# Kernel optimization log

Hardware: AMD Instinct MI355X
Metric: run time of the kernel (lower is better)

## Reference

```python
import jax, jax.numpy as jnp
import numpy as np

DIM = 2560; HEADS = 20; HEAD_DIM = 128
N_EXP = 4; TOP_K = 2; HID = 6912; SHID = 3584
B = 1; S = 2048
EPS = 1e-6


def setup_inputs():
    key = jax.random.key(0)
    ks = jax.random.split(key, 16)
    r = lambda i, shape, s=0.02: jax.random.normal(ks[i], shape, jnp.float32) * s
    # rope as [1,S,1,HD/2,2,2] rotation matrices: [[cos,-sin],[sin,cos]]
    ang = jax.random.uniform(ks[0], (1, S, 1, HEAD_DIM // 2), jnp.float32) * (2.0 * np.pi)
    c, s_ = jnp.cos(ang), jnp.sin(ang)
    rope = jnp.stack([jnp.stack([c, -s_], -1), jnp.stack([s_, c], -1)], -2)
    return dict(
        hidden_states=jax.random.normal(ks[1], (B, S, DIM), jnp.float32),
        temb=jax.random.normal(ks[2], (B, DIM), jnp.float32),
        rope=rope,
        adaln_w=r(3, (6 * DIM, DIM)), adaln_b=jnp.zeros((6 * DIM,), jnp.float32),
        qkv_w=r(4, (3 * DIM, DIM)), qkv_b=jnp.zeros((3 * DIM,), jnp.float32),
        qn_w=jnp.ones((DIM,), jnp.float32), kn_w=jnp.ones((DIM,), jnp.float32),
        out_w=r(5, (DIM, DIM)), out_b=jnp.zeros((DIM,), jnp.float32),
        gate_w=r(6, (N_EXP, DIM), 1.0 / DIM ** 0.5),
        ew1=r(7, (N_EXP, HID, DIM)), ew2=r(8, (N_EXP, DIM, HID)), ew3=r(9, (N_EXP, HID, DIM)),
        sw1=r(10, (SHID, DIM)), sw2=r(11, (DIM, SHID)), sw3=r(12, (SHID, DIM)),
    )


def _layernorm(x):  # elementwise_affine=False, eps=1e-6
    m = x.mean(-1, keepdims=True)
    v = ((x - m) ** 2).mean(-1, keepdims=True)
    return (x - m) * jax.lax.rsqrt(v + EPS)


def _rmsnorm(x, w):  # DistributedRMSNorm, tp_size=1
    return x * jax.lax.rsqrt((x ** 2).mean(-1, keepdims=True) + EPS) * w


def _apply_rope(x, rope):  # x:[B,S,H,D], rope:[1,S,1,D/2,2,2]
    b, s, h, d = x.shape
    x_ = x.reshape(b, s, h, d // 2, 1, 2)
    out = rope[..., 0] * x_[..., 0] + rope[..., 1] * x_[..., 1]  # [B,S,H,D/2,2]
    return out.reshape(b, s, h, d)


def _swiglu(x, w1, w2, w3):
    return (jax.nn.silu(x @ w1.T) * (x @ w3.T)) @ w2.T


def _forward(hidden_states, temb, rope, adaln_w, adaln_b, qkv_w, qkv_b, qn_w, kn_w,
             out_w, out_b, gate_w, ew1, ew2, ew3, sw1, sw2, sw3):
    b, s, d = hidden_states.shape
    # adaLN modulation: SiLU -> Linear -> [:, None] -> chunk(6)
    mod = (jax.nn.silu(temb) @ adaln_w.T + adaln_b)[:, None, :]
    shift_msa, scale_msa, gate_msa, shift_mlp, scale_mlp, gate_mlp = jnp.split(mod, 6, axis=-1)
    # --- attention ---
    nh = _layernorm(hidden_states) * (1.0 + scale_msa) + shift_msa
    qkv = nh @ qkv_w.T + qkv_b
    q, k, v = jnp.split(qkv, 3, axis=-1)  # each [B,S,inner_dim]
    q = _rmsnorm(q, qn_w)  # RMS over full inner_dim (all heads)
    k = _rmsnorm(k, kn_w)
    q = q.reshape(b, s, HEADS, HEAD_DIM)
    k = k.reshape(b, s, HEADS, HEAD_DIM)
    v = v.reshape(b, s, HEADS, HEAD_DIM)
    q = _apply_rope(q, rope)
    k = _apply_rope(k, rope)
    attn = jnp.einsum('bqhd,bkhd->bhqk', q, k) * (HEAD_DIM ** -0.5)
    attn = jax.nn.softmax(attn, axis=-1)
    o = jnp.einsum('bhqk,bkhd->bqhd', attn, v).reshape(b, s, HEADS * HEAD_DIM)
    o = o @ out_w.T + out_b
    hidden_states = gate_msa * o + hidden_states
    # --- MoE SwiGLU feed-forward ---
    nh = _layernorm(hidden_states) * (1.0 + scale_mlp) + shift_mlp
    x = nh.reshape(-1, d)  # [T,d]
    scores = jax.nn.softmax(x @ gate_w.T, axis=-1)  # [T,E]
    tw, ti = jax.lax.top_k(scores, TOP_K)  # norm_topk_prob=False
    t = x.shape[0]
    wdense = jnp.zeros((t, N_EXP), x.dtype).at[jnp.arange(t)[:, None], ti].set(tw)
    y = jnp.zeros_like(x)
    for e in range(N_EXP):  # fixed small expert count
        y = y + wdense[:, e:e + 1] * _swiglu(x, ew1[e], ew2[e], ew3[e])
    y = y.reshape(b, s, d) + _swiglu(nh, sw1, sw2, sw3)  # shared experts on identity
    return gate_mlp * y + hidden_states


def reference(hidden_states, temb, rope, adaln_w, adaln_b, qkv_w, qkv_b, qn_w, kn_w,
              out_w, out_b, gate_w, ew1, ew2, ew3, sw1, sw2, sw3):
    return _forward(hidden_states, temb, rope, adaln_w, adaln_b, qkv_w, qkv_b, qn_w, kn_w,
                    out_w, out_b, gate_w, ew1, ew2, ew3, sw1, sw2, sw3)
```

## Files before the change

kernel.cpp:

```cpp
#include <hip/hip_runtime.h>

#define DIM 2560
#define T_TOK 2048
#define NHEADS 20
#define HD 128
#define HID_E 6912
#define SHID_E 3584
#define MPAD 5120

typedef _Float16 f16x8 __attribute__((ext_vector_type(8)));
typedef float f32x4 __attribute__((ext_vector_type(4)));
typedef unsigned short u16x8 __attribute__((ext_vector_type(8)));

#define MFMA16(a, b, c) __builtin_amdgcn_mfma_f32_16x16x32_f16((a), (b), (c), 0, 0, 0)

__device__ inline unsigned short f2h(float f) {
  return __builtin_bit_cast(unsigned short, (_Float16)f);
}
__device__ inline float h2f(unsigned short u) {
  return (float)__builtin_bit_cast(_Float16, u);
}
__device__ inline float wave_sum(float v) {
#pragma unroll
  for (int off = 32; off > 0; off >>= 1) v += __shfl_down(v, off, 64);
  return v;
}
__device__ inline void gld16(const void* g, void* l) {
  __builtin_amdgcn_global_load_lds((const __attribute__((address_space(1))) void*)g,
                                   (__attribute__((address_space(3))) void*)l, 16, 0, 0);
}


__global__ __launch_bounds__(256) void silu_k(const float* __restrict__ t,
                                              float* __restrict__ ss) {
  int i = blockIdx.x * 256 + threadIdx.x;
  if (i < DIM) {
    float v = t[i];
    ss[i] = v / (1.f + expf(-v));
  }
}

__global__ __launch_bounds__(256) void cvt_all2(
    const float* __restrict__ s0, unsigned short* __restrict__ d0, long n0,
    const float* __restrict__ s1, unsigned short* __restrict__ d1, long n1) {
  const long stride = (long)gridDim.x * 256;
  const long tot = n0 + n1;
  for (long i = (long)blockIdx.x * 256 + threadIdx.x; i < tot; i += stride) {
    const float* s;
    unsigned short* d;
    long j;
    if (i < n0) { s = s0; d = d0; j = i; }
    else { s = s1; d = d1; j = i - n0; }
    float4 a = *(const float4*)(s + j * 8);
    float4 b = *(const float4*)(s + j * 8 + 4);
    u16x8 u;
    u[0] = f2h(a.x); u[1] = f2h(a.y); u[2] = f2h(a.z); u[3] = f2h(a.w);
    u[4] = f2h(b.x); u[5] = f2h(b.y); u[6] = f2h(b.z); u[7] = f2h(b.w);
    *(u16x8*)&d[j * 8] = u;
  }
}

__global__ __launch_bounds__(256) void adaln_gemv(const float* __restrict__ ss,
                                                  const float* __restrict__ W,
                                                  const float* __restrict__ bias,
                                                  float* __restrict__ mod) {
  const int lane = threadIdx.x & 63;
  const int j = blockIdx.x * 4 + (threadIdx.x >> 6);
  const float* wr = W + (size_t)j * DIM;
  float p = 0.f;
  for (int i = lane; i < 640; i += 64) {
    float4 w = *(const float4*)(wr + i * 4);
    float4 x = *(const float4*)(ss + i * 4);
    p += w.x * x.x + w.y * x.y + w.z * x.z + w.w * x.w;
  }
  p = wave_sum(p);
  if (lane == 0) mod[j] = p + bias[j];
}

__global__ __launch_bounds__(256) void ln_mod(const float* __restrict__ x,
                                              const float* __restrict__ shift,
                                              const float* __restrict__ scale,
                                              unsigned short* __restrict__ outp) {
  __shared__ float rbuf[8];
  const int t = blockIdx.x, tid = threadIdx.x, lane = tid & 63, wid = tid >> 6;
  const float* xr = x + (size_t)t * DIM;
  float s = 0.f, sq = 0.f;
  for (int i = tid; i < 640; i += 256) {
    float4 v = *(const float4*)(xr + i * 4);
    s += v.x + v.y + v.z + v.w;
    sq += v.x * v.x + v.y * v.y + v.z * v.z + v.w * v.w;
  }
  s = wave_sum(s);
  sq = wave_sum(sq);
  if (lane == 0) {
    rbuf[wid] = s;
    rbuf[4 + wid] = sq;
  }
  __syncthreads();
  float S = rbuf[0] + rbuf[1] + rbuf[2] + rbuf[3];
  float SQ = rbuf[4] + rbuf[5] + rbuf[6] + rbuf[7];
  float mean = S * (1.f / DIM);
  float rs = rsqrtf(SQ * (1.f / DIM) - mean * mean + 1e-6f);
  for (int i = tid; i < 640; i += 256) {
    float4 v = *(const float4*)(xr + i * 4);
    float4 sc4 = *(const float4*)(scale + i * 4);
    float4 sh4 = *(const float4*)(shift + i * 4);
    ushort4 u;
    u.x = f2h((v.x - mean) * rs * (1.f + sc4.x) + sh4.x);
    u.y = f2h((v.y - mean) * rs * (1.f + sc4.y) + sh4.y);
    u.z = f2h((v.z - mean) * rs * (1.f + sc4.z) + sh4.z);
    u.w = f2h((v.w - mean) * rs * (1.f + sc4.w) + sh4.w);
    *(ushort4*)&outp[(size_t)t * DIM + i * 4] = u;
  }
}

__global__ __launch_bounds__(256) void rmsrope(const unsigned short* __restrict__ qkv,
                                               const float* __restrict__ qn,
                                               const float* __restrict__ kn,
                                               const float* __restrict__ rope,
                                               unsigned short* __restrict__ qh,
                                               unsigned short* __restrict__ kh) {
  __shared__ float rbuf[8];
  const int t = blockIdx.x, tid = threadIdx.x, lane = tid & 63, wid = tid >> 6;
  const unsigned short* row = qkv + (size_t)t * 7680;
  float sq = 0.f, sk = 0.f;
  for (int i = tid; i < 320; i += 256) {
    f16x8 qv = *(const f16x8*)(row + i * 8);
    f16x8 kv = *(const f16x8*)(row + DIM + i * 8);
#pragma unroll
    for (int j = 0; j < 8; ++j) {
      float q = (float)qv[j], k = (float)kv[j];
      sq += q * q;
      sk += k * k;
    }
  }
  sq = wave_sum(sq);
  sk = wave_sum(sk);
  if (lane == 0) {
    rbuf[wid] = sq;
    rbuf[4 + wid] = sk;
  }
  __syncthreads();
  float SQ = rbuf[0] + rbuf[1] + rbuf[2] + rbuf[3];
  float SK = rbuf[4] + rbuf[5] + rbuf[6] + rbuf[7];
  float rq = rsqrtf(SQ * (1.f / DIM) + 1e-6f) * 0.08838834764831845f;
  float rk = rsqrtf(SK * (1.f / DIM) + 1e-6f);
  for (int pp = tid; pp < 1280; pp += 256) {
    int c = pp * 2;
    float qe = h2f(row[c]) * rq * qn[c], qo = h2f(row[c + 1]) * rq * qn[c + 1];
    float ke = h2f(row[DIM + c]) * rk * kn[c], ko = h2f(row[DIM + c + 1]) * rk * kn[c + 1];
    float4 rr = *(const float4*)(rope + (size_t)t * 256 + (pp & 63) * 4);
    unsigned qp = (unsigned)f2h(rr.x * qe + rr.y * qo) |
                  ((unsigned)f2h(rr.z * qe + rr.w * qo) << 16);
    unsigned kp = (unsigned)f2h(rr.x * ke + rr.y * ko) |
                  ((unsigned)f2h(rr.z * ke + rr.w * ko) << 16);
    *(unsigned*)&qh[(size_t)t * DIM + c] = qp;
    *(unsigned*)&kh[(size_t)t * DIM + c] = kp;
  }
}

__global__ void transpose_v(const unsigned short* __restrict__ in,
                            unsigned short* __restrict__ outp) {
  __shared__ unsigned short tile[32][33];
  const int bx = blockIdx.x * 32;
  const int by = blockIdx.y * 32;
  const int tx = threadIdx.x, ty = threadIdx.y;
  for (int j = ty; j < 32; j += 8)
    tile[j][tx] = in[(size_t)(by + j) * 7680 + 5120 + bx + tx];
  __syncthreads();
  for (int j = ty; j < 32; j += 8)
    outp[(size_t)(bx + j) * T_TOK + by + tx] = tile[tx][j];
}

__global__ __launch_bounds__(256) void fattn(const unsigned short* __restrict__ qh,
                                             const unsigned short* __restrict__ kh,
                                             const unsigned short* __restrict__ vt,
                                             unsigned short* __restrict__ obuf) {
  __shared__ unsigned short sK[64 * 128];
  __shared__ unsigned short sV[128 * 64];
  __shared__ unsigned short sP[64 * 64];
  __shared__ float sRedM[4][64];
  __shared__ float sRedL[4][64];
  __shared__ float sM[64];
  __shared__ float sL[64];
  const int tid = threadIdx.x, lane = tid & 63, wv = tid >> 6;
  const int g = lane >> 4, fr = lane & 15;
  const int h = blockIdx.y;
  const int q0 = blockIdx.x * 64;

  {
    const int r = tid >> 2, qt = tid & 3;
    const unsigned short* gp = qh + (size_t)(q0 + r) * DIM + h * HD + qt * 32;
    uint4 v0 = ((const uint4*)gp)[0];
    uint4 v1 = ((const uint4*)gp)[1];
    uint4 v2 = ((const uint4*)gp)[2];
    uint4 v3 = ((const uint4*)gp)[3];
    unsigned short* dst = &sK[r * 128];
    const int cb = qt * 4, rs = r & 15;
    *(uint4*)&dst[((cb + 0) ^ rs) * 8] = v0;
    *(uint4*)&dst[((cb + 1) ^ rs) * 8] = v1;
    *(uint4*)&dst[((cb + 2) ^ rs) * 8] = v2;
    *(uint4*)&dst[((cb + 3) ^ rs) * 8] = v3;
  }
  __syncthreads();
  f16x8 qfrag[4][4];
#pragma unroll
  for (int ni = 0; ni < 4; ++ni) {
#pragma unroll
    for (int kt = 0; kt < 4; ++kt) {
      int r = ni * 16 + fr;
      qfrag[ni][kt] = *(const f16x8*)&sK[r * 128 + (((kt * 4 + g) ^ (r & 15)) << 3)];
    }
  }
  __syncthreads();

  f32x4 acco[4][2];
  f32x4 mprev[4];
  float mrun[4], lrun[4];
#pragma unroll
  for (int i = 0; i < 4; ++i) {
    acco[i][0] = (f32x4)0.f;
    acco[i][1] = (f32x4)0.f;
    mprev[i] = (f32x4)(-1e30f);
    mrun[i] = -1e30f;
    lrun[i] = 0.f;
  }

  for (int kt0 = 0; kt0 < T_TOK; kt0 += 64) {
    {
      const int r = tid >> 2, qt = tid & 3;
      const unsigned short* gp = kh + (size_t)(kt0 + r) * DIM + h * HD + qt * 32;
      uint4 v0 = ((const uint4*)gp)[0];
      uint4 v1 = ((const uint4*)gp)[1];
      uint4 v2 = ((const uint4*)gp)[2];
      uint4 v3 = ((const uint4*)gp)[3];
      unsigned short* dst = &sK[r * 128];
      const int cb = qt * 4, rs = r & 15;
      *(uint4*)&dst[((cb + 0) ^ rs) * 8] = v0;
      *(uint4*)&dst[((cb + 1) ^ rs) * 8] = v1;
      *(uint4*)&dst[((cb + 2) ^ rs) * 8] = v2;
      *(uint4*)&dst[((cb + 3) ^ rs) * 8] = v3;
      const int rv = tid >> 1, hf = tid & 1;
      const unsigned short* gv = vt + (size_t)(h * HD + rv) * T_TOK + kt0 + hf * 32;
      uint4 w0 = ((const uint4*)gv)[0];
      uint4 w1 = ((const uint4*)gv)[1];
      uint4 w2 = ((const uint4*)gv)[2];
      uint4 w3 = ((const uint4*)gv)[3];
      unsigned short* dv = &sV[rv * 64];
      const int cv = hf * 4, rvs = rv & 7;
      *(uint4*)&dv[((cv + 0) ^ rvs) * 8] = w0;
      *(uint4*)&dv[((cv + 1) ^ rvs) * 8] = w1;
      *(uint4*)&dv[((cv + 2) ^ rvs) * 8] = w2;
      *(uint4*)&dv[((cv + 3) ^ rvs) * 8] = w3;
    }
    __syncthreads();

    f32x4 accs[4] = {(f32x4)0.f, (f32x4)0.f, (f32x4)0.f, (f32x4)0.f};
#pragma unroll
    for (int kt = 0; kt < 4; ++kt) {
      int r = wv * 16 + fr;
      f16x8 ak = *(const f16x8*)&sK[r * 128 + (((kt * 4 + g) ^ (r & 15)) << 3)];
#pragma unroll
      for (int ni = 0; ni < 4; ++ni) accs[ni] = MFMA16(ak, qfrag[ni][kt], accs[ni]);
    }

    float pm[4];
#pragma unroll
    for (int ni = 0; ni < 4; ++ni) {
      float m = fmaxf(fmaxf(accs[ni][0], accs[ni][1]), fmaxf(accs[ni][2], accs[ni][3]));
      m = fmaxf(m, __shfl_xor(m, 16));
      m = fmaxf(m, __shfl_xor(m, 32));
      pm[ni] = m;
    }
    if (g == 0) {
#pragma unroll
      for (int ni = 0; ni < 4; ++ni) sRedM[wv][ni * 16 + fr] = pm[ni];
    }
    __syncthreads();
    float mnew[4];
#pragma unroll
    for (int ni = 0; ni < 4; ++ni) {
      int q = ni * 16 + fr;
      float mt = fmaxf(fmaxf(sRedM[0][q], sRedM[1][q]), fmaxf(sRedM[2][q], sRedM[3][q]));
      mnew[ni] = fmaxf(mrun[ni], mt);
    }
    float lsum[4];
#pragma unroll
    for (int ni = 0; ni < 4; ++ni) {
      float l0 = 0.f;
#pragma unroll
      for (int i = 0; i < 4; ++i) {
        float p = __expf(accs[ni][i] - mnew[ni]);
        accs[ni][i] = p;
        l0 += p;
      }
      l0 += __shfl_xor(l0, 16);
      l0 += __shfl_xor(l0, 32);
      lsum[ni] = l0;
    }
    if (g == 0) {
#pragma unroll
      for (int ni = 0; ni < 4; ++ni) sRedL[wv][ni * 16 + fr] = lsum[ni];
      if (wv == 0) {
#pragma unroll
        for (int ni = 0; ni < 4; ++ni) sM[ni * 16 + fr] = mnew[ni];
      }
    }
#pragma unroll
    for (int ni = 0; ni < 4; ++ni) {
      int q = ni * 16 + fr;
      unsigned p01 = (unsigned)f2h(accs[ni][0]) | ((unsigned)f2h(accs[ni][1]) << 16);
      unsigned p23 = (unsigned)f2h(accs[ni][2]) | ((unsigned)f2h(accs[ni][3]) << 16);
      uint2 pk;
      pk.x = p01;
      pk.y = p23;
      *(uint2*)&sP[q * 64 + ((((wv << 1) | (g >> 1)) ^ (q & 7)) << 3) + ((g & 1) << 2)] = pk;
    }
    __syncthreads();
#pragma unroll
    for (int ni = 0; ni < 4; ++ni) {
      int q = ni * 16 + fr;
      float lt = sRedL[0][q] + sRedL[1][q] + sRedL[2][q] + sRedL[3][q];
      lrun[ni] = lrun[ni] * __expf(mrun[ni] - mnew[ni]) + lt;
      mrun[ni] = mnew[ni];
    }

#pragma unroll
    for (int mi = 0; mi < 4; ++mi) {
      f32x4 mn = *(const f32x4*)&sM[mi * 16 + g * 4];
      f32x4 sc;
#pragma unroll
      for (int i = 0; i < 4; ++i) sc[i] = __expf(mprev[mi][i] - mn[i]);
      acco[mi][0] *= sc;
      acco[mi][1] *= sc;
      mprev[mi] = mn;
    }
#pragma unroll
    for (int ktp = 0; ktp < 2; ++ktp) {
      f16x8 bv[2];
#pragma unroll
      for (int nd = 0; nd < 2; ++nd) {
        int r = wv * 32 + nd * 16 + fr;
        bv[nd] = *(const f16x8*)&sV[r * 64 + (((ktp * 4 + g) ^ (r & 7)) << 3)];
      }
#pragma unroll
      for (int mi = 0; mi < 4; ++mi) {
        int r = mi * 16 + fr;
        f16x8 ap = *(const f16x8*)&sP[r * 64 + (((ktp * 4 + g) ^ (r & 7)) << 3)];
        acco[mi][0] = MFMA16(ap, bv[0], acco[mi][0]);
        acco[mi][1] = MFMA16(ap, bv[1], acco[mi][1]);
      }
    }
    __syncthreads();
  }

  if (wv == 0 && g == 0) {
#pragma unroll
    for (int ni = 0; ni < 4; ++ni) sL[ni * 16 + fr] = 1.f / lrun[ni];
  }
  __syncthreads();
#pragma unroll
  for (int mi = 0; mi < 4; ++mi) {
    f32x4 li = *(const f32x4*)&sL[mi * 16 + g * 4];
#pragma unroll
    for (int nd = 0; nd < 2; ++nd) {
#pragma unroll
      for (int i = 0; i < 4; ++i) {
        float o = acco[mi][nd][i] * li[i];
        obuf[(size_t)(q0 + mi * 16 + g * 4 + i) * DIM + h * HD + wv * 32 + nd * 16 + fr] =
            f2h(o);
      }
    }
  }
}

__global__ __launch_bounds__(256) void ln2_route(const float* __restrict__ x,
                                                 const float* __restrict__ shift,
                                                 const float* __restrict__ scale,
                                                 const float* __restrict__ gw,
                                                 unsigned short* __restrict__ nh2,
                                                 float* __restrict__ wd) {
  __shared__ float rbuf[8];
  __shared__ float gbuf[4][4];
  const int t = blockIdx.x, tid = threadIdx.x, lane = tid & 63, wid = tid >> 6;
  const float* xr = x + (size_t)t * DIM;
  float s = 0.f, sq = 0.f;
  for (int i = tid; i < 640; i += 256) {
    float4 v = *(const float4*)(xr + i * 4);
    s += v.x + v.y + v.z + v.w;
    sq += v.x * v.x + v.y * v.y + v.z * v.z + v.w * v.w;
  }
  s = wave_sum(s);
  sq = wave_sum(sq);
  if (lane == 0) {
    rbuf[wid] = s;
    rbuf[4 + wid] = sq;
  }
  __syncthreads();
  float S = rbuf[0] + rbuf[1] + rbuf[2] + rbuf[3];
  float SQ = rbuf[4] + rbuf[5] + rbuf[6] + rbuf[7];
  float mean = S * (1.f / DIM);
  float rs = rsqrtf(SQ * (1.f / DIM) - mean * mean + 1e-6f);
  float g0 = 0.f, g1 = 0.f, g2 = 0.f, g3 = 0.f;
  for (int i = tid; i < 640; i += 256) {
    float4 v = *(const float4*)(xr + i * 4);
    float4 sc4 = *(const float4*)(scale + i * 4);
    float4 sh4 = *(const float4*)(shift + i * 4);
    float y0 = (v.x - mean) * rs * (1.f + sc4.x) + sh4.x;
    float y1 = (v.y - mean) * rs * (1.f + sc4.y) + sh4.y;
    float y2 = (v.z - mean) * rs * (1.f + sc4.z) + sh4.z;
    float y3 = (v.w - mean) * rs * (1.f + sc4.w) + sh4.w;
    ushort4 u;
    u.x = f2h(y0); u.y = f2h(y1); u.z = f2h(y2); u.w = f2h(y3);
    *(ushort4*)&nh2[(size_t)t * DIM + i * 4] = u;
    float4 w0 = *(const float4*)(gw + i * 4);
    float4 w1 = *(const float4*)(gw + DIM + i * 4);
    float4 w2 = *(const float4*)(gw + 2 * DIM + i * 4);
    float4 w3 = *(const float4*)(gw + 3 * DIM + i * 4);
    g0 += y0 * w0.x + y1 * w0.y + y2 * w0.z + y3 * w0.w;
    g1 += y0 * w1.x + y1 * w1.y + y2 * w1.z + y3 * w1.w;
    g2 += y0 * w2.x + y1 * w2.y + y2 * w2.z + y3 * w2.w;
    g3 += y0 * w3.x + y1 * w3.y + y2 * w3.z + y3 * w3.w;
  }
  g0 = wave_sum(g0);
  g1 = wave_sum(g1);
  g2 = wave_sum(g2);
  g3 = wave_sum(g3);
  if (lane == 0) {
    gbuf[wid][0] = g0; gbuf[wid][1] = g1; gbuf[wid][2] = g2; gbuf[wid][3] = g3;
  }
  __syncthreads();
  if (tid == 0) {
    float l[4];
#pragma unroll
    for (int e = 0; e < 4; ++e) l[e] = gbuf[0][e] + gbuf[1][e] + gbuf[2][e] + gbuf[3][e];
    float mx = fmaxf(fmaxf(l[0], l[1]), fmaxf(l[2], l[3]));
    float ex[4], sum = 0.f;
#pragma unroll
    for (int e = 0; e < 4; ++e) { ex[e] = expf(l[e] - mx); sum += ex[e]; }
    float p[4];
#pragma unroll
    for (int e = 0; e < 4; ++e) p[e] = ex[e] / sum;
    int i1 = 0;
    for (int e = 1; e < 4; ++e)
      if (p[e] > p[i1]) i1 = e;
    int i2 = -1;
    for (int e = 0; e < 4; ++e) {
      if (e == i1) continue;
      if (i2 < 0 || p[e] > p[i2]) i2 = e;
    }
    float w[4] = {0.f, 0.f, 0.f, 0.f};
    w[i1] = p[i1];
    w[i2] = p[i2];
    *(float4*)&wd[(size_t)t * 4] = make_float4(w[0], w[1], w[2], w[3]);
  }
}

__global__ __launch_bounds__(256) void route_compact(const float* __restrict__ wd,
                                                     int* __restrict__ idx_all,
                                                     int* __restrict__ seg,
                                                     int* __restrict__ slotAB,
                                                     float* __restrict__ wAB) {
  __shared__ unsigned short c[256][4];
  __shared__ int offs[256][4];
  __shared__ int segs[5];
  const int t = threadIdx.x;
  for (int i = t; i < MPAD; i += 256) idx_all[i] = 0;
  unsigned char sel[8];
  float wv4[8][4];
  unsigned short lc[4] = {0, 0, 0, 0};
#pragma unroll
  for (int k = 0; k < 8; ++k) {
    int tok = t * 8 + k;
    float4 w = *(const float4*)&wd[(size_t)tok * 4];
    wv4[k][0] = w.x; wv4[k][1] = w.y; wv4[k][2] = w.z; wv4[k][3] = w.w;
    unsigned m = 0;
    if (w.x != 0.f) { m |= 1; lc[0]++; }
    if (w.y != 0.f) { m |= 2; lc[1]++; }
    if (w.z != 0.f) { m |= 4; lc[2]++; }
    if (w.w != 0.f) { m |= 8; lc[3]++; }
    sel[k] = (unsigned char)m;
  }
#pragma unroll
  for (int e = 0; e < 4; ++e) c[t][e] = lc[e];
  __syncthreads();
  if (t == 0) {
    int run[4] = {0, 0, 0, 0};
    for (int i = 0; i < 256; ++i) {
#pragma unroll
      for (int e = 0; e < 4; ++e) {
        offs[i][e] = run[e];
        run[e] += c[i][e];
      }
    }
    int s = 0;
    segs[0] = 0;
#pragma unroll
    for (int e = 0; e < 4; ++e) {
      s += (run[e] + 255) & ~255;
      segs[e + 1] = s;
    }
#pragma unroll
    for (int e = 0; e < 5; ++e) seg[e] = segs[e];
  }
  __syncthreads();
  int o[4];
#pragma unroll
  for (int e = 0; e < 4; ++e) o[e] = segs[e] + offs[t][e];
#pragma unroll
  for (int k = 0; k < 8; ++k) {
    int tok = t * 8 + k;
    unsigned m = sel[k];
    int sl[2] = {0, 0};
    float sw[2] = {0.f, 0.f};
    int ns = 0;
#pragma unroll
    for (int e = 0; e < 4; ++e) {
      if ((m >> e) & 1) {
        if (ns < 2) { sl[ns] = o[e]; sw[ns] = wv4[k][e]; }
        idx_all[o[e]++] = tok;
        ns++;
      }
    }
    if (ns == 1) { sl[1] = sl[0]; sw[1] = 0.f; }
    slotAB[tok * 2] = sl[0];
    slotAB[tok * 2 + 1] = sl[1];
    wAB[tok * 2] = sw[0];
    wAB[tok * 2 + 1] = sw[1];
  }
}

template <int EPI, int MODE>
__global__ __launch_bounds__(256) void gemm128(
    const unsigned short* __restrict__ A, const unsigned short* __restrict__ B,
    const float* __restrict__ bias, void* __restrict__ Cv,
    const float* __restrict__ aux0, const float* __restrict__ aux1,
    const int* __restrict__ idx, const int* __restrict__ seg,
    const int* __restrict__ slotAB, const float* __restrict__ wAB,
    const unsigned short* __restrict__ yc, int M, int N, int K) {
  __shared__ unsigned short smem[16384];
  const int tid = threadIdx.x;
  const int lane = tid & 63;
  const int wv = tid >> 6;
  const int nwg = gridDim.x;
  const int bid = blockIdx.x;
  const int swzb = (bid & 7) * (nwg >> 3) + (bid >> 3);
  const int gm = M >> 7;
  const int m0 = (swzb % gm) * 128, n0 = (swzb / gm) * 128;
  if (MODE != 0 && m0 >= seg[4]) return;

  const unsigned short* Bp = B;
  if constexpr (MODE != 0) {
    int e = 0;
#pragma unroll
    for (int i = 1; i < 4; ++i)
      if (m0 >= seg[i]) e = i;
    Bp = B + (size_t)e * N * K;
  }

  const int wm = (wv >> 1) * 64, wn = (wv & 1) * 64;
  const int fr = lane & 15, fc = lane >> 4;

  const int rl = lane >> 2, ch = lane & 3;
  const int R1 = wv * 16 + rl;
  const int R2 = 64 + R1;
  const int co1 = ((ch ^ ((R1 >> 1) & 3)) << 3);
  const int co2 = ((ch ^ ((R2 >> 1) & 3)) << 3);
  const size_t ar1 = (size_t)(m0 + R1) * K;
  const size_t ar2 = (size_t)(m0 + R2) * K;
  const unsigned short* gA1 = A + ar1 + co1;
  const unsigned short* gA2 = A + ar2 + co2;
  const unsigned short* gB1 = Bp + (size_t)(n0 + R1) * K + co1;
  const unsigned short* gB2 = Bp + (size_t)(n0 + R2) * K + co2;
  const int lA1 = (wv * 16) * 32, lA2 = (64 + wv * 16) * 32;

  f32x4 acc[4][4];
#pragma unroll
  for (int i = 0; i < 4; ++i) {
#pragma unroll
    for (int j = 0; j < 4; ++j) acc[i][j] = (f32x4)0.f;
  }

  auto STAGE = [&](int buf, int kt) {
    unsigned short* base = smem + buf * 8192;
    gld16(gA1 + kt, base + lA1);
    gld16(gA2 + kt, base + lA2);
    gld16(gB1 + kt, base + 4096 + lA1);
    gld16(gB2 + kt, base + 4096 + lA2);
  };
  auto COMPUTE = [&](int buf) {
    const unsigned short* sA = smem + buf * 8192;
    const unsigned short* sB = sA + 4096;
    f16x8 a[4], b[4];
#pragma unroll
    for (int mi = 0; mi < 4; ++mi) {
      int r = wm + mi * 16 + fr;
      a[mi] = *(const f16x8*)&sA[r * 32 + ((fc ^ ((r >> 1) & 3)) << 3)];
    }
#pragma unroll
    for (int ni = 0; ni < 4; ++ni) {
      int r = wn + ni * 16 + fr;
      b[ni] = *(const f16x8*)&sB[r * 32 + ((fc ^ ((r >> 1) & 3)) << 3)];
    }
#pragma unroll
    for (int mi = 0; mi < 4; ++mi) {
#pragma unroll
      for (int ni = 0; ni < 4; ++ni) acc[mi][ni] = MFMA16(a[mi], b[ni], acc[mi][ni]);
    }
  };

  const int nk = K >> 5;
  STAGE(0, 0);
  __syncthreads();
  int cur = 0;
  for (int t = 1; t < nk; ++t) {
    STAGE(cur ^ 1, t << 5);
    COMPUTE(cur);
    __syncthreads();
    cur ^= 1;
  }
  COMPUTE(cur);

#pragma unroll
  for (int mi = 0; mi < 4; ++mi) {
#pragma unroll
    for (int ni = 0; ni < 4; ++ni) {
      const int n = n0 + wn + ni * 16 + fr;
      const int mb = m0 + wm + mi * 16 + fc * 4;
#pragma unroll
      for (int i = 0; i < 4; ++i) {
        const int m = mb + i;
        float v = acc[mi][ni][i];
        const size_t cidx = (size_t)m * N + n;
        if constexpr (EPI == 1) {
          ((float*)Cv)[cidx] = aux0[n] * (v + bias[n]) + aux1[cidx];
        } else if constexpr (EPI == 4) {
          if (bias) v += bias[n];
          ((unsigned short*)Cv)[cidx] = f2h(v);
        } else if constexpr (EPI == 6) {
          const int sA_ = slotAB[m * 2], sB_ = slotAB[m * 2 + 1];
          const float wA_ = wAB[m * 2], wB_ = wAB[m * 2 + 1];
          float vm = wA_ * h2f(yc[(size_t)sA_ * N + n]) + wB_ * h2f(yc[(size_t)sB_ * N + n]);
          ((float*)Cv)[cidx] = aux0[n] * (v + vm) + aux1[cidx];
        }
      }
    }
  }
}

template <int EPI, int MODE, int PAIR>
__global__ __launch_bounds__(512) void gemm256(
    const unsigned short* __restrict__ A, const float* __restrict__ B1,
    const float* __restrict__ B3, const float* __restrict__ bias,
    void* __restrict__ Cv, const int* __restrict__ idx, const int* __restrict__ seg,
    int M, int N, int K) {
  __shared__ __align__(16) char smem[147456];
  const int tid = threadIdx.x;
  const int lane = tid & 63;
  const int wv = tid >> 6;
  const int wr = wv >> 2;
  const int wc = wv & 3;
  const int fr = lane & 15, fc = lane >> 4;

  const int nwg = gridDim.x;
  const int bid = blockIdx.x;
  const int swzb = (bid & 7) * (nwg >> 3) + (bid >> 3);
  const int gm = M >> 8;
  const int m0 = (swzb % gm) * 256, n0 = (swzb / gm) * 256;
  if (MODE != 0 && m0 >= seg[4]) return;

  const float* B1p = B1;
  const float* B3p = B3;
  if constexpr (MODE != 0) {
    int e = 0;
#pragma unroll
    for (int i = 1; i < 4; ++i)
      if (m0 >= seg[i]) e = i;
    if constexpr (PAIR) {
      B1p = B1 + (size_t)e * (N >> 1) * K;
      B3p = B3 + (size_t)e * (N >> 1) * K;
    } else {
      B1p = B1 + (size_t)e * N * K;
    }
  }

  const int srowA = lane >> 2;
  const int sccA = ((lane & 3) ^ ((lane >> 3) & 3)) << 3;
  int mr0, mr1;
  if constexpr (MODE == 1) {
    mr0 = idx[m0 + wv * 16 + srowA];
    mr1 = idx[m0 + 128 + wv * 16 + srowA];
  } else {
    mr0 = m0 + wv * 16 + srowA;
    mr1 = m0 + 128 + wv * 16 + srowA;
  }
  const unsigned short* gA0 = A + (size_t)mr0 * K + sccA;
  const unsigned short* gA1 = A + (size_t)mr1 * K + sccA;

  const int srowB = lane >> 3;
  const int sccB = ((lane & 7) ^ srowB) << 2;
  const float* gB[4];
#pragma unroll
  for (int s = 0; s < 4; ++s) {
    const int rB = n0 + wv * 32 + s * 8 + srowB;
    const float* bsrc;
    if constexpr (PAIR) {
      const float* mptr = ((rB >> 4) & 1) ? B3p : B1p;
      bsrc = mptr + (size_t)((rB >> 5) * 16 + (rB & 15)) * K;
    } else {
      bsrc = B1p + (size_t)rB * K;
    }
    gB[s] = bsrc + sccB;
  }

  const int swA_ = (fr >> 1) & 3;
  const int foA = ((fc ^ swA_) << 3);
  const int aoff = (wr * 128 + fr) * 32 + foA;
  const int mB = fr & 7;
  const int bc0 = ((2 * fc) ^ mB) << 2;
  const int bc1 = ((2 * fc + 1) ^ mB) << 2;

  f32x4 acc[8][4];
#pragma unroll
  for (int i = 0; i < 8; ++i) {
#pragma unroll
    for (int j = 0; j < 4; ++j) acc[i][j] = (f32x4)0.f;
  }

  auto STAGE_A = [&](int buf, int kt) {
    char* bb = smem + buf * 49152;
    gld16(gA0 + kt, bb + wv * 1024);
    gld16(gA1 + kt, bb + 8192 + wv * 1024);
  };
  auto STAGE_B = [&](int buf, int kt) {
    char* bb = smem + buf * 49152 + 16384 + wv * 4096;
#pragma unroll
    for (int s = 0; s < 4; ++s) gld16(gB[s] + kt, bb + s * 1024);
  };

  const int nk = K >> 5;
  STAGE_A(0, 0);
  STAGE_B(0, 0);
  STAGE_A(1, 32);
  STAGE_B(1, 32);

  int cur = 0;
  for (int t = 0; t < nk; ++t) {
    if (t < nk - 1)
      asm volatile("s_waitcnt vmcnt(6)" ::: "memory");
    else
      asm volatile("s_waitcnt vmcnt(0)" ::: "memory");
    __builtin_amdgcn_s_barrier();
    __builtin_amdgcn_sched_barrier(0);

    const unsigned short* sA = (const unsigned short*)(smem + cur * 49152);
    const float* sB = (const float*)(smem + cur * 49152 + 16384);
    int nxt = cur + 2;
    if (nxt >= 3) nxt -= 3;
    const bool more = (t + 2) < nk;
    const int kn = (t + 2) << 5;

    f16x8 bfr[4];
#pragma unroll
    for (int ni = 0; ni < 4; ++ni) {
      const float* rowp = sB + (wc * 64 + ni * 16 + fr) * 32;
      float4 x = *(const float4*)&rowp[bc0];
      float4 y = *(const float4*)&rowp[bc1];
      f16x8 b;
      b[0] = (_Float16)x.x; b[1] = (_Float16)x.y; b[2] = (_Float16)x.z; b[3] = (_Float16)x.w;
      b[4] = (_Float16)y.x; b[5] = (_Float16)y.y; b[6] = (_Float16)y.z; b[7] = (_Float16)y.w;
      bfr[ni] = b;
    }
    f16x8 b0 = bfr[0], b1 = bfr[1], b2 = bfr[2], b3 = bfr[3];

    {
      f16x8 a0 = *(const f16x8*)&sA[aoff];
      f16x8 a1 = *(const f16x8*)&sA[aoff + 512];
      if (more) STAGE_A(nxt, kn);
      __builtin_amdgcn_sched_barrier(0);
      __builtin_amdgcn_s_setprio(1);
      acc[0][0] = MFMA16(a0, b0, acc[0][0]);
      acc[0][1] = MFMA16(a0, b1, acc[0][1]);
      acc[0][2] = MFMA16(a0, b2, acc[0][2]);
      acc[0][3] = MFMA16(a0, b3, acc[0][3]);
      acc[1][0] = MFMA16(a1, b0, acc[1][0]);
      acc[1][1] = MFMA16(a1, b1, acc[1][1]);
      acc[1][2] = MFMA16(a1, b2, acc[1][2]);
      acc[1][3] = MFMA16(a1, b3, acc[1][3]);
      __builtin_amdgcn_s_setprio(0);
      __builtin_amdgcn_sched_barrier(0);
    }
    {
      f16x8 a0 = *(const f16x8*)&sA[aoff + 1024];
      f16x8 a1 = *(const f16x8*)&sA[aoff + 1536];
      if (more) STAGE_B(nxt, kn);
      __builtin_amdgcn_sched_barrier(0);
      __builtin_amdgcn_s_setprio(1);
      acc[2][0] = MFMA16(a0, b0, acc[2][0]);
      acc[2][1] = MFMA16(a0, b1, acc[2][1]);
      acc[2][2] = MFMA16(a0, b2, acc[2][2]);
      acc[2][3] = MFMA16(a0, b3, acc[2][3]);
      acc[3][0] = MFMA16(a1, b0, acc[3][0]);
      acc[3][1] = MFMA16(a1, b1, acc[3][1]);
      acc[3][2] = MFMA16(a1, b2, acc[3][2]);
      acc[3][3] = MFMA16(a1, b3, acc[3][3]);
      __builtin_amdgcn_s_setprio(0);
      __builtin_amdgcn_sched_barrier(0);
    }
    {
      f16x8 a0 = *(const f16x8*)&sA[aoff + 2048];
      f16x8 a1 = *(const f16x8*)&sA[aoff + 2560];
      __builtin_amdgcn_sched_barrier(0);
      __builtin_amdgcn_s_setprio(1);
      acc[4][0] = MFMA16(a0, b0, acc[4][0]);
      acc[4][1] = MFMA16(a0, b1, acc[4][1]);
      acc[4][2] = MFMA16(a0, b2, acc[4][2]);
      acc[4][3] = MFMA16(a0, b3, acc[4][3]);
      acc[5][0] = MFMA16(a1, b0, acc[5][0]);
      acc[5][1] = MFMA16(a1, b1, acc[5][1]);
      acc[5][2] = MFMA16(a1, b2, acc[5][2]);
      acc[5][3] = MFMA16(a1, b3, acc[5][3]);
      __builtin_amdgcn_s_setprio(0);
      __builtin_amdgcn_sched_barrier(0);
    }
    {
      f16x8 a0 = *(const f16x8*)&sA[aoff + 3072];
      f16x8 a1 = *(const f16x8*)&sA[aoff + 3584];
      __builtin_amdgcn_sched_barrier(0);
      __builtin_amdgcn_s_setprio(1);
      acc[6][0] = MFMA16(a0, b0, acc[6][0]);
      acc[6][1] = MFMA16(a0, b1, acc[6][1]);
      acc[6][2] = MFMA16(a0, b2, acc[6][2]);
      acc[6][3] = MFMA16(a0, b3, acc[6][3]);
      acc[7][0] = MFMA16(a1, b0, acc[7][0]);
      acc[7][1] = MFMA16(a1, b1, acc[7][1]);
      acc[7][2] = MFMA16(a1, b2, acc[7][2]);
      acc[7][3] = MFMA16(a1, b3, acc[7][3]);
      __builtin_amdgcn_s_setprio(0);
      __builtin_amdgcn_sched_barrier(0);
    }
    cur += 1;
    if (cur >= 3) cur -= 3;
  }

  if constexpr (EPI == 5) {
    unsigned short* Ch = (unsigned short*)Cv;
    const int Nh = N >> 1;
#pragma unroll
    for (int mi = 0; mi < 8; ++mi) {
#pragma unroll
      for (int p = 0; p < 2; ++p) {
        const int hcol = (((n0 + wc * 64) >> 5) + p) * 16 + fr;
        const int mb = m0 + wr * 128 + mi * 16 + fc * 4;
#pragma unroll
        for (int i = 0; i < 4; ++i) {
          const int m = mb + i;
          float v1 = acc[mi][2 * p][i];
          float v3 = acc[mi][2 * p + 1][i];
          float y = v1 / (1.f + __expf(-v1)) * v3;
          Ch[(size_t)m * Nh + hcol] = f2h(y);
        }
      }
    }
  } else {
    unsigned short* Ch = (unsigned short*)Cv;
#pragma unroll
    for (int mi = 0; mi < 8; ++mi) {
#pragma unroll
      for (int ni = 0; ni < 4; ++ni) {
        const int n = n0 + wc * 64 + ni * 16 + fr;
        const int mb = m0 + wr * 128 + mi * 16 + fc * 4;
#pragma unroll
        for (int i = 0; i < 4; ++i) {
          const int m = mb + i;
          float v = acc[mi][ni][i];
          if (bias) v += bias[n];
          Ch[(size_t)m * N + n] = f2h(v);
        }
      }
    }
  }
}


extern "C" void kernel_launch(void* const* d_in, const int* in_sizes, int n_in,
                              void* d_out, int out_size, void* d_ws, size_t ws_size,
                              hipStream_t stream) {
  (void)in_sizes; (void)n_in; (void)out_size; (void)ws_size;
  const float* hs = (const float*)d_in[0];
  const float* temb = (const float*)d_in[1];
  const float* rope = (const float*)d_in[2];
  const float* adaw = (const float*)d_in[3];
  const float* adab = (const float*)d_in[4];
  const float* qkvw = (const float*)d_in[5];
  const float* qkvb = (const float*)d_in[6];
  const float* qnw = (const float*)d_in[7];
  const float* knw = (const float*)d_in[8];
  const float* outw = (const float*)d_in[9];
  const float* outb = (const float*)d_in[10];
  const float* gatew = (const float*)d_in[11];
  const float* ew1 = (const float*)d_in[12];
  const float* ew2 = (const float*)d_in[13];
  const float* ew3 = (const float*)d_in[14];
  const float* sw1 = (const float*)d_in[15];
  const float* sw2 = (const float*)d_in[16];
  const float* sw3 = (const float*)d_in[17];
  float* out = (float*)d_out;
  char* ws = (char*)d_ws;

  size_t off = 0;
  auto give = [&](size_t nbytes) {
    size_t r = off;
    off += (nbytes + 255) & ~(size_t)255;
    return r;
  };
  const size_t T = T_TOK, D = DIM;
  size_t o_mod = give(15360 * 4);
  size_t o_ss = give(D * 4);
  size_t o_wd = give(T * 4 * 4);
  size_t o_idx = give(MPAD * 4);
  size_t o_seg = give(8 * 4);
  size_t o_slot = give(T * 2 * 4);
  size_t o_wab = give(T * 2 * 4);
  size_t o_nh = give(T * D * 2);
  size_t o_qkvh = give(T * 7680 * 2);
  size_t o_qh = give(T * D * 2);
  size_t o_kh = give(T * D * 2);
  size_t o_vt = give(T * D * 2);
  size_t o_obf = give(T * D * 2);
  size_t o_h2 = give(T * D * 4);
  size_t o_yc = give((size_t)MPAD * D * 2);
  size_t o_hmid2 = give(T * SHID_E * 2);
  size_t o_outw = give((size_t)2560 * 2560 * 2);
  size_t o_sw2 = give((size_t)2560 * SHID_E * 2);

  float* mod = (float*)(ws + o_mod);
  float* ss = (float*)(ws + o_ss);
  float* wd = (float*)(ws + o_wd);
  int* idxb = (int*)(ws + o_idx);
  int* segp = (int*)(ws + o_seg);
  int* slotAB = (int*)(ws + o_slot);
  float* wAB = (float*)(ws + o_wab);
  unsigned short* nh_h = (unsigned short*)(ws + o_nh);
  unsigned short* qkvh = (unsigned short*)(ws + o_qkvh);
  unsigned short* qh = (unsigned short*)(ws + o_qh);
  unsigned short* kh = (unsigned short*)(ws + o_kh);
  unsigned short* vt = (unsigned short*)(ws + o_vt);
  unsigned short* obf = (unsigned short*)(ws + o_obf);
  float* h2 = (float*)(ws + o_h2);
  unsigned short* yc = (unsigned short*)(ws + o_yc);
  unsigned short* hmid2 = (unsigned short*)(ws + o_hmid2);
  unsigned short* outw_h = (unsigned short*)(ws + o_outw);
  unsigned short* sw2_h = (unsigned short*)(ws + o_sw2);
  unsigned short* nh2 = nh_h;
  unsigned short* hmid = qkvh;

  cvt_all2<<<2048, 256, 0, stream>>>(outw, outw_h, 2560L * 2560 / 8,
                                     sw2, sw2_h, 2560L * SHID_E / 8);
  silu_k<<<10, 256, 0, stream>>>(temb, ss);
  adaln_gemv<<<3840, 256, 0, stream>>>(ss, adaw, adab, mod);
  ln_mod<<<T, 256, 0, stream>>>(hs, mod, mod + D, nh_h);
  gemm256<4, 0, 0><<<240, 512, 0, stream>>>(nh_h, qkvw, nullptr, qkvb, qkvh,
                                            nullptr, nullptr, 2048, 7680, 2560);
  rmsrope<<<T, 256, 0, stream>>>(qkvh, qnw, knw, rope, qh, kh);
  transpose_v<<<dim3(80, 64), dim3(32, 8), 0, stream>>>(qkvh, vt);
  fattn<<<dim3(32, 20), 256, 0, stream>>>(qh, kh, vt, obf);
  gemm128<1, 0><<<16 * 20, 256, 0, stream>>>(obf, outw_h, outb, h2,
                                             mod + 2 * D, hs, nullptr, nullptr,
                                             nullptr, nullptr, nullptr, 2048, 2560, 2560);
  ln2_route<<<T, 256, 0, stream>>>(h2, mod + 3 * D, mod + 4 * D, gatew, nh2, wd);
  route_compact<<<1, 256, 0, stream>>>(wd, idxb, segp, slotAB, wAB);
  gemm256<5, 1, 1><<<20 * 54, 512, 0, stream>>>(nh2, ew1, ew3, nullptr, hmid,
                                                idxb, segp, MPAD, 2 * HID_E, 2560);
  gemm256<4, 2, 0><<<20 * 10, 512, 0, stream>>>(hmid, ew2, nullptr, nullptr, yc,
                                                nullptr, segp, MPAD, 2560, 6912);
  gemm256<5, 0, 1><<<8 * 28, 512, 0, stream>>>(nh2, sw1, sw3, nullptr, hmid2,
                                               nullptr, nullptr, 2048, 2 * SHID_E, 2560);
  gemm128<6, 0><<<16 * 20, 256, 0, stream>>>(hmid2, sw2_h, nullptr, out,
                                             mod + 5 * D, h2, nullptr, nullptr,
                                             slotAB, wAB, yc, 2048, 2560, 3584);
}
```

Measured before the change: 1.344 ms.

## Convert fp32 B tiles to fp16 once via registers before LDS store in gemm256

The 256x256 GEMM now loads fp32 weight tiles into registers, converts them to fp16 once, and stores them into a double-buffered fp16 LDS region. Before, raw fp32 was staged into LDS with async loads and each wave converted after reading. This halves LDS size and traffic for B (smem drops from 147KB to 80KB) and removes repeated per-wave conversions, which could allow more occupancy. The cost is that the register-staged global loads are synchronous, so the conversion and LDS write sit at the end of each k-step and add waits and register pressure.

```diff
diff --git a/kernel.cpp b/kernel.cpp
--- a/kernel.cpp
+++ b/kernel.cpp
@@ -654,7 +654,7 @@
     const float* __restrict__ B3, const float* __restrict__ bias,
     void* __restrict__ Cv, const int* __restrict__ idx, const int* __restrict__ seg,
     int M, int N, int K) {
-  __shared__ __align__(16) char smem[147456];
+  __shared__ __align__(16) char smem[81920];
   const int tid = threadIdx.x;
   const int lane = tid & 63;
   const int wv = tid >> 6;
@@ -697,12 +697,12 @@
   const unsigned short* gA0 = A + (size_t)mr0 * K + sccA;
   const unsigned short* gA1 = A + (size_t)mr1 * K + sccA;
 
-  const int srowB = lane >> 3;
-  const int sccB = ((lane & 7) ^ srowB) << 2;
-  const float* gB[4];
-#pragma unroll
-  for (int s = 0; s < 4; ++s) {
-    const int rB = n0 + wv * 32 + s * 8 + srowB;
+  const float* gB[2];
+  unsigned wrOff[2];
+#pragma unroll
+  for (int sp = 0; sp < 2; ++sp) {
+    const int rloc = wv * 32 + sp * 16 + (lane >> 2);
+    const int rB = n0 + rloc;
     const float* bsrc;
     if constexpr (PAIR) {
       const float* mptr = ((rB >> 4) & 1) ? B3p : B1p;
@@ -710,15 +710,14 @@
     } else {
       bsrc = B1p + (size_t)rB * K;
     }
-    gB[s] = bsrc + sccB;
-  }
-
-  const int swA_ = (fr >> 1) & 3;
-  const int foA = ((fc ^ swA_) << 3);
+    gB[sp] = bsrc + (lane & 3) * 8;
+    const int cl = (lane & 3) ^ ((rloc >> 1) & 3);
+    wrOff[sp] = (unsigned)(rloc * 64 + cl * 16);
+  }
+
+  const int foA = ((fc ^ ((fr >> 1) & 3)) << 3);
   const int aoff = (wr * 128 + fr) * 32 + foA;
-  const int mB = fr & 7;
-  const int bc0 = ((2 * fc) ^ mB) << 2;
-  const int bc1 = ((2 * fc + 1) ^ mB) << 2;
+  const int boff0 = (wc * 64 + fr) * 32 + foA;
 
   f32x4 acc[8][4];
 #pragma unroll
@@ -728,55 +727,62 @@
   }
 
   auto STAGE_A = [&](int buf, int kt) {
-    char* bb = smem + buf * 49152;
+    char* bb = smem + buf * 16384;
     gld16(gA0 + kt, bb + wv * 1024);
     gld16(gA1 + kt, bb + 8192 + wv * 1024);
   };
-  auto STAGE_B = [&](int buf, int kt) {
-    char* bb = smem + buf * 49152 + 16384 + wv * 4096;
-#pragma unroll
-    for (int s = 0; s < 4; ++s) gld16(gB[s] + kt, bb + s * 1024);
-  };
 
   const int nk = K >> 5;
   STAGE_A(0, 0);
-  STAGE_B(0, 0);
   STAGE_A(1, 32);
-  STAGE_B(1, 32);
-
-  int cur = 0;
+  {
+    float4 p0a = *(const float4*)(gB[0]);
+    float4 p0b = *(const float4*)(gB[0] + 4);
+    float4 p1a = *(const float4*)(gB[1]);
+    float4 p1b = *(const float4*)(gB[1] + 4);
+    asm volatile("s_waitcnt vmcnt(0)" ::: "memory");
+    f16x8 h0, h1;
+    h0[0] = (_Float16)p0a.x; h0[1] = (_Float16)p0a.y; h0[2] = (_Float16)p0a.z; h0[3] = (_Float16)p0a.w;
+    h0[4] = (_Float16)p0b.x; h0[5] = (_Float16)p0b.y; h0[6] = (_Float16)p0b.z; h0[7] = (_Float16)p0b.w;
+    h1[0] = (_Float16)p1a.x; h1[1] = (_Float16)p1a.y; h1[2] = (_Float16)p1a.z; h1[3] = (_Float16)p1a.w;
+    h1[4] = (_Float16)p1b.x; h1[5] = (_Float16)p1b.y; h1[6] = (_Float16)p1b.z; h1[7] = (_Float16)p1b.w;
+    *(f16x8*)(smem + 49152 + wrOff[0]) = h0;
+    *(f16x8*)(smem + 49152 + wrOff[1]) = h1;
+  }
+
+  int curA = 0;
   for (int t = 0; t < nk; ++t) {
-    if (t < nk - 1)
-      asm volatile("s_waitcnt vmcnt(6)" ::: "memory");
-    else
-      asm volatile("s_waitcnt vmcnt(0)" ::: "memory");
+    asm volatile("s_waitcnt lgkmcnt(0)" ::: "memory");
     __builtin_amdgcn_s_barrier();
     __builtin_amdgcn_sched_barrier(0);
 
-    const unsigned short* sA = (const unsigned short*)(smem + cur * 49152);
-    const float* sB = (const float*)(smem + cur * 49152 + 16384);
-    int nxt = cur + 2;
-    if (nxt >= 3) nxt -= 3;
-    const bool more = (t + 2) < nk;
-    const int kn = (t + 2) << 5;
-
-    f16x8 bfr[4];
-#pragma unroll
-    for (int ni = 0; ni < 4; ++ni) {
-      const float* rowp = sB + (wc * 64 + ni * 16 + fr) * 32;
-      float4 x = *(const float4*)&rowp[bc0];
-      float4 y = *(const float4*)&rowp[bc1];
-      f16x8 b;
-      b[0] = (_Float16)x.x; b[1] = (_Float16)x.y; b[2] = (_Float16)x.z; b[3] = (_Float16)x.w;
-      b[4] = (_Float16)y.x; b[5] = (_Float16)y.y; b[6] = (_Float16)y.z; b[7] = (_Float16)y.w;
-      bfr[ni] = b;
-    }
-    f16x8 b0 = bfr[0], b1 = bfr[1], b2 = bfr[2], b3 = bfr[3];
+    const unsigned short* sA = (const unsigned short*)(smem + curA * 16384);
+    const unsigned short* sB = (const unsigned short*)(smem + 49152 + (t & 1) * 16384);
+    int nxtA = curA + 2;
+    if (nxtA >= 3) nxtA -= 3;
+    const bool more1 = (t + 1) < nk;
+    const bool more2 = (t + 2) < nk;
+    const int k1 = (t + 1) << 5;
+    const int k2 = (t + 2) << 5;
+
+    f16x8 b0 = *(const f16x8*)&sB[boff0];
+    f16x8 b1 = *(const f16x8*)&sB[boff0 + 512];
+    f16x8 b2 = *(const f16x8*)&sB[boff0 + 1024];
+    f16x8 b3 = *(const f16x8*)&sB[boff0 + 1536];
+
+    float4 p0a, p0b, p1a, p1b;
+    if (more1) {
+      p0a = *(const float4*)(gB[0] + k1);
+      p0b = *(const float4*)(gB[0] + k1 + 4);
+      p1a = *(const float4*)(gB[1] + k1);
+      p1b = *(const float4*)(gB[1] + k1 + 4);
+    }
+    __builtin_amdgcn_sched_barrier(0);
 
     {
       f16x8 a0 = *(const f16x8*)&sA[aoff];
       f16x8 a1 = *(const f16x8*)&sA[aoff + 512];
-      if (more) STAGE_A(nxt, kn);
+      if (more2) STAGE_A(nxtA, k2);
       __builtin_amdgcn_sched_barrier(0);
       __builtin_amdgcn_s_setprio(1);
       acc[0][0] = MFMA16(a0, b0, acc[0][0]);
@@ -793,7 +799,6 @@
     {
       f16x8 a0 = *(const f16x8*)&sA[aoff + 1024];
       f16x8 a1 = *(const f16x8*)&sA[aoff + 1536];
-      if (more) STAGE_B(nxt, kn);
       __builtin_amdgcn_sched_barrier(0);
       __builtin_amdgcn_s_setprio(1);
       acc[2][0] = MFMA16(a0, b0, acc[2][0]);
@@ -839,8 +844,24 @@
       __builtin_amdgcn_s_setprio(0);
       __builtin_amdgcn_sched_barrier(0);
     }
-    cur += 1;
-    if (cur >= 3) cur -= 3;
+
+    if (more1) {
+      if (more2)
+        asm volatile("s_waitcnt vmcnt(2)" ::: "memory");
+      else
+        asm volatile("s_waitcnt vmcnt(0)" ::: "memory");
+      __builtin_amdgcn_sched_barrier(0);
+      f16x8 h0, h1;
+      h0[0] = (_Float16)p0a.x; h0[1] = (_Float16)p0a.y; h0[2] = (_Float16)p0a.z; h0[3] = (_Float16)p0a.w;
+      h0[4] = (_Float16)p0b.x; h0[5] = (_Float16)p0b.y; h0[6] = (_Float16)p0b.z; h0[7] = (_Float16)p0b.w;
+      h1[0] = (_Float16)p1a.x; h1[1] = (_Float16)p1a.y; h1[2] = (_Float16)p1a.z; h1[3] = (_Float16)p1a.w;
+      h1[4] = (_Float16)p1b.x; h1[5] = (_Float16)p1b.y; h1[6] = (_Float16)p1b.z; h1[7] = (_Float16)p1b.w;
+      char* bb = smem + 49152 + ((t + 1) & 1) * 16384;
+      *(f16x8*)(bb + wrOff[0]) = h0;
+      *(f16x8*)(bb + wrOff[1]) = h1;
+    }
+    curA += 1;
+    if (curA >= 3) curA -= 3;
   }
 
   if constexpr (EPI == 5) {
```

Measured after the change: 1.759 ms. 30.8% more time.
